# Performance work log

Measured on AMD Instinct MI355X. Metric: run time of the kernel, lower is better.

The kernel has to match this reference:

```python
import jax, jax.numpy as jnp
import numpy as np

NUM_ROWS = 125000
NUM_CACHE = 100000
EMB_DIMS = 128
ROW = [50, 50, 50]
EMB = [4, 4, 8]
R = [1, 32, 32, 1]
TT_IDX = jnp.array([2500, 50, 1], dtype=jnp.int64)  # strides from create_tt_idx_shape
NUM_IDX = 204800
NUM_BAGS = 4096


def setup_inputs() -> dict:
    key = jax.random.key(0)
    ks = jax.random.split(key, 8)
    indices = jax.random.randint(ks[0], (NUM_IDX,), 0, NUM_ROWS, dtype=jnp.int64)
    offsets = jnp.sort(jax.random.randint(ks[1], (NUM_BAGS + 1,), 0, NUM_IDX, dtype=jnp.int64))
    offsets = offsets.at[0].set(0).at[-1].set(NUM_IDX)
    cached_indices = jax.random.randint(ks[2], (NUM_IDX,), 0, NUM_CACHE, dtype=jnp.int64)
    cached_offsets = jnp.sort(jax.random.randint(ks[3], (NUM_BAGS + 1,), 0, NUM_IDX, dtype=jnp.int64))
    cached_offsets = cached_offsets.at[0].set(0).at[-1].set(NUM_IDX)
    sigma = 1.0 / np.sqrt(NUM_ROWS)
    core0 = jax.random.normal(ks[4], (ROW[0], R[0] * EMB[0] * R[1]), dtype=jnp.float32) * sigma
    core1 = jax.random.normal(ks[5], (ROW[1], R[1] * EMB[1] * R[2]), dtype=jnp.float32) * sigma
    core2 = jax.random.normal(ks[6], (ROW[2], R[2] * EMB[2] * R[3]), dtype=jnp.float32) * sigma
    cache_table = jax.random.normal(ks[7], (NUM_CACHE, EMB_DIMS), dtype=jnp.float32)
    return {"indices": indices, "offsets": offsets, "cached_indices": cached_indices,
            "cached_offsets": cached_offsets, "core0": core0, "core1": core1,
            "core2": core2, "cache_table": cache_table}


def _bag_ids(offsets, n):
    # bag id for each flat index position (include_last_offset convention)
    return jnp.searchsorted(offsets, jnp.arange(n, dtype=offsets.dtype), side='right') - 1


def reference(indices, offsets, cached_indices, cached_offsets, core0, core1, core2, cache_table):
    n = indices.shape[0]
    # TT index digit decomposition
    d0 = (indices // TT_IDX[0]) % ROW[0]
    d1 = (indices // TT_IDX[1]) % ROW[1]
    d2 = (indices // TT_IDX[2]) % ROW[2]
    g0 = core0[d0].reshape(n, EMB[0], R[1])            # [n, e0, r1]
    g1 = core1[d1].reshape(n, R[1], EMB[1], R[2])      # [n, r1, e1, r2]
    g2 = core2[d2].reshape(n, R[2], EMB[2])            # [n, r2, e2]
    t = jnp.einsum('nxr,nrys->nxys', g0, g1).reshape(n, EMB[0] * EMB[1], R[2])
    emb = jnp.einsum('nkr,nrz->nkz', t, g2).reshape(n, EMB_DIMS)  # [n, 128]
    seg_tt = _bag_ids(offsets, n)
    tt_bag = jax.ops.segment_sum(emb, seg_tt, num_segments=NUM_BAGS)
    seg_c = _bag_ids(cached_offsets, cached_indices.shape[0])
    cache_bag = jax.ops.segment_sum(cache_table[cached_indices], seg_c, num_segments=NUM_BAGS)
    return cache_bag + tt_bag
```

## Files before the change

### kernel.cpp

```cpp
#include <hip/hip_runtime.h>
#include <hip/hip_bf16.h>


#define PAIRS 2500
#define CHT 64
#define CHC 32

typedef unsigned int u32;
typedef unsigned short u16;

__device__ __forceinline__ float bfu(u16 u) { return __uint_as_float(((u32)u) << 16); }
__device__ __forceinline__ u16 f2bf(float x) {
  __hip_bfloat16 h = __float2bfloat16(x);
  return *reinterpret_cast<u16*>(&h);
}

__device__ __forceinline__ void gload_lds16(const void* g, void* l) {
  __builtin_amdgcn_global_load_lds(
      (const __attribute__((address_space(1))) u32*)g,
      (__attribute__((address_space(3))) u32*)l, 16, 0, 0);
}

__global__ __launch_bounds__(256) void chat_kernel(const float* __restrict__ core2,
                                                   float* __restrict__ chat) {
  const int d2 = blockIdx.x;
  const int tid = threadIdx.x;
  const int r = tid >> 3, z = tid & 7;
  chat[d2 * 288 + z * 36 + r] = core2[d2 * 256 + r * 8 + z];
}

__global__ __launch_bounds__(512, 4) void build_emb_kernel(
    const float* __restrict__ core0, const float* __restrict__ core1,
    const float* __restrict__ chat, u16* __restrict__ emb_t) {
  __shared__ float c0s[128];
  __shared__ float c1s[4096];
  __shared__ float ts[512];
  const int p = blockIdx.x;
  const int d0 = p / 50, d1 = p - d0 * 50;
  const int tid = threadIdx.x;

  {
    const float4* s1 = reinterpret_cast<const float4*>(core1 + (size_t)d1 * 4096);
    float4* dst = reinterpret_cast<float4*>(c1s);
    dst[tid] = s1[tid];
    dst[tid + 512] = s1[tid + 512];
    if (tid < 32)
      reinterpret_cast<float4*>(c0s)[tid] =
          reinterpret_cast<const float4*>(core0 + (size_t)d0 * 128)[tid];
  }
  __syncthreads();

  {
    const int kk = tid >> 5, s = tid & 31;
    const int x = kk >> 2, y = kk & 3;
    float acc = 0.f;
#pragma unroll
    for (int r = 0; r < 32; ++r)
      acc += c0s[x * 32 + r] * c1s[r * 128 + y * 32 + s];
    ts[kk * 32 + s] = acc;
  }
  __syncthreads();

  if (tid < 400) {
    const int d2 = tid >> 3, z = tid & 7;
    float4 c[8];
    const float4* cp = reinterpret_cast<const float4*>(chat + d2 * 288 + z * 36);
#pragma unroll
    for (int rq = 0; rq < 8; ++rq) c[rq] = cp[rq];
    const float4* t4 = reinterpret_cast<const float4*>(ts);
    u16* op = emb_t + (((size_t)(p * 50 + d2)) << 7) + z;
#pragma unroll
    for (int kk = 0; kk < 16; ++kk) {
      float s = 0.f;
#pragma unroll
      for (int rq = 0; rq < 8; ++rq) {
        const float4 tb = t4[kk * 8 + rq];
        s += tb.x * c[rq].x + tb.y * c[rq].y + tb.z * c[rq].z + tb.w * c[rq].w;
      }
      op[kk * 8] = f2bf(s);
    }
  }
}

__device__ __forceinline__ int bag_search(const int* __restrict__ offs,
                                          int nbags, int p) {
  int lo = 0, hi = nbags;
  while (hi - lo > 1) {
    int m = (lo + hi) >> 1;
    if (offs[m] <= p) lo = m; else hi = m;
  }
  return lo;
}

__global__ __launch_bounds__(256, 8) void sum_kernel(
    const int* __restrict__ indices, const int* __restrict__ offsets,
    const int* __restrict__ cached_indices, const int* __restrict__ cached_offsets,
    const float* __restrict__ cache_table, const u16* __restrict__ emb_t,
    float* __restrict__ out, int n, int nbags, int ntt_blocks) {
  __shared__ __align__(16) u16 sdat[CHT * 128];
  __shared__ int sidx[CHT];
  __shared__ int sbag[CHT];
  const int tid = threadIdx.x;
  const int bid = blockIdx.x;
  const int lane = tid & 63;
  const int w = tid >> 6;

  if (bid < ntt_blocks) {
    const int base = bid * CHT;
    const int count = min(CHT, n - base);
    if (tid < count) {
      sidx[tid] = indices[base + tid];
      sbag[tid] = bag_search(offsets, nbags, base + tid);
    }
    __syncthreads();
    if (count == CHT) {
      u32* ldsb = reinterpret_cast<u32*>(sdat);
#pragma unroll
      for (int j = 0; j < 4; ++j) {
        const int r4 = w * 16 + j * 4;
        const int row = r4 + (lane >> 4);
        const char* src = reinterpret_cast<const char*>(emb_t) +
                          (((size_t)sidx[row]) << 8) + ((lane & 15) << 4);
        gload_lds16(src, ldsb + r4 * 64);
      }
    } else {
      for (int r = w; r < count; r += 4) {
        reinterpret_cast<u32*>(sdat)[r * 64 + lane] =
            reinterpret_cast<const u32*>(emb_t)[(((size_t)sidx[r]) << 6) + lane];
      }
    }
    __syncthreads();
    const int k = tid & 127, h = tid >> 7;
    const int rlo = h * (CHT / 2);
    const int rhi = min(count, rlo + CHT / 2);
    float acc = 0.f;
    for (int i = rlo; i < rhi; ++i) {
      acc += bfu(sdat[i * 128 + k]);
      if (i + 1 == rhi || sbag[i + 1] != sbag[i]) {
        atomicAdd(out + (((size_t)sbag[i]) << 7) + k, acc);
        acc = 0.f;
      }
    }
  } else {
    const int cb = bid - ntt_blocks;
    const int base = cb * CHC;
    const int count = min(CHC, n - base);
    float* sfl = reinterpret_cast<float*>(sdat);
    if (tid < count) {
      sidx[tid] = cached_indices[base + tid];
      sbag[tid] = bag_search(cached_offsets, nbags, base + tid);
    }
    __syncthreads();
    if (count == CHC) {
#pragma unroll
      for (int j = 0; j < 4; ++j) {
        const int r2 = w * 8 + j * 2;
        const int row = r2 + (lane >> 5);
        const char* src = reinterpret_cast<const char*>(cache_table) +
                          (((size_t)sidx[row]) << 9) + ((lane & 31) << 4);
        gload_lds16(src, sfl + r2 * 128);
      }
    } else {
      for (int r = w; r < count; r += 4) {
        reinterpret_cast<float2*>(sfl + r * 128)[lane] =
            reinterpret_cast<const float2*>(cache_table + (((size_t)sidx[r]) << 7))[lane];
      }
    }
    __syncthreads();
    const int k = tid & 127, h = tid >> 7;
    const int rlo = h * (CHC / 2);
    const int rhi = min(count, rlo + CHC / 2);
    float acc = 0.f;
    for (int i = rlo; i < rhi; ++i) {
      acc += sfl[i * 128 + k];
      if (i + 1 == rhi || sbag[i + 1] != sbag[i]) {
        atomicAdd(out + (((size_t)sbag[i]) << 7) + k, acc);
        acc = 0.f;
      }
    }
  }
}

extern "C" void kernel_launch(void* const* d_in, const int* in_sizes, int n_in,
                              void* d_out, int out_size, void* d_ws, size_t ws_size,
                              hipStream_t stream) {
  const int* indices        = (const int*)d_in[0];
  const int* offsets        = (const int*)d_in[1];
  const int* cached_indices = (const int*)d_in[2];
  const int* cached_offsets = (const int*)d_in[3];
  const float* core0        = (const float*)d_in[4];
  const float* core1        = (const float*)d_in[5];
  const float* core2        = (const float*)d_in[6];
  const float* cache_table  = (const float*)d_in[7];
  float* out = (float*)d_out;

  const int n = in_sizes[0];
  const int nbags = in_sizes[1] - 1;

  u16* emb_t = (u16*)d_ws;
  float* chat = (float*)((char*)d_ws + 32000000);

  hipMemsetAsync(out, 0, (size_t)out_size * sizeof(float), stream);

  chat_kernel<<<50, 256, 0, stream>>>(core2, chat);
  build_emb_kernel<<<PAIRS, 512, 0, stream>>>(core0, core1, chat, emb_t);

  const int ntt = (n + CHT - 1) / CHT;
  const int nc  = (n + CHC - 1) / CHC;
  sum_kernel<<<ntt + nc, 256, 0, stream>>>(
      indices, offsets, cached_indices, cached_offsets, cache_table, emb_t,
      out, n, nbags, ntt);
}
```

Before: 165.9 us.

## Stage embedding tiles in swizzled LDS, overlap index loads with bag search

The build kernel now writes each pair's 50x128 bf16 block into a swizzled shared buffer and copies it out with coalesced 8-byte stores, replacing the strided 2-byte global stores. It also loads the core2 coefficients before the first barrier and removes the padded stride. The sum kernel reads indices straight from global memory so the gathers are issued before the bag binary search, precomputes a per-row bag/end flag, and has each thread accumulate two columns over quarter-chunks. This roughly doubles the number of atomics per row segment and adds extra shared memory and barriers in exchange for better store coalescing and load/search overlap.

Measured after the change: 193.6 us. 1.17x slower.

```diff
diff --git a/kernel.cpp b/kernel.cpp
--- a/kernel.cpp
+++ b/kernel.cpp
@@ -9,7 +9,8 @@
 typedef unsigned int u32;
 typedef unsigned short u16;
 
-__device__ __forceinline__ float bfu(u16 u) { return __uint_as_float(((u32)u) << 16); }
+__device__ __forceinline__ float bflo(u32 u) { return __uint_as_float(u << 16); }
+__device__ __forceinline__ float bfhi(u32 u) { return __uint_as_float(u & 0xffff0000u); }
 __device__ __forceinline__ u16 f2bf(float x) {
   __hip_bfloat16 h = __float2bfloat16(x);
   return *reinterpret_cast<u16*>(&h);
@@ -26,7 +27,7 @@
   const int d2 = blockIdx.x;
   const int tid = threadIdx.x;
   const int r = tid >> 3, z = tid & 7;
-  chat[d2 * 288 + z * 36 + r] = core2[d2 * 256 + r * 8 + z];
+  chat[d2 * 256 + z * 32 + r] = core2[d2 * 256 + r * 8 + z];
 }
 
 __global__ __launch_bounds__(512, 4) void build_emb_kernel(
@@ -35,6 +36,7 @@
   __shared__ float c0s[128];
   __shared__ float c1s[4096];
   __shared__ float ts[512];
+  __shared__ __align__(16) u16 ebuf[6400];
   const int p = blockIdx.x;
   const int d0 = p / 50, d1 = p - d0 * 50;
   const int tid = threadIdx.x;
@@ -48,6 +50,14 @@
       reinterpret_cast<float4*>(c0s)[tid] =
           reinterpret_cast<const float4*>(core0 + (size_t)d0 * 128)[tid];
   }
+
+  const int d2 = tid >> 3, z = tid & 7;
+  float4 c[8];
+  if (tid < 400) {
+    const float4* cp = reinterpret_cast<const float4*>(chat + d2 * 256 + z * 32);
+#pragma unroll
+    for (int rq = 0; rq < 8; ++rq) c[rq] = cp[rq];
+  }
   __syncthreads();
 
   {
@@ -62,13 +72,8 @@
   __syncthreads();
 
   if (tid < 400) {
-    const int d2 = tid >> 3, z = tid & 7;
-    float4 c[8];
-    const float4* cp = reinterpret_cast<const float4*>(chat + d2 * 288 + z * 36);
-#pragma unroll
-    for (int rq = 0; rq < 8; ++rq) c[rq] = cp[rq];
     const float4* t4 = reinterpret_cast<const float4*>(ts);
-    u16* op = emb_t + (((size_t)(p * 50 + d2)) << 7) + z;
+    const u32 sw = ((u32)(d2 & 7)) << 4;
 #pragma unroll
     for (int kk = 0; kk < 16; ++kk) {
       float s = 0.f;
@@ -77,7 +82,19 @@
         const float4 tb = t4[kk * 8 + rq];
         s += tb.x * c[rq].x + tb.y * c[rq].y + tb.z * c[rq].z + tb.w * c[rq].w;
       }
-      op[kk * 8] = f2bf(s);
+      const u32 byte = (u32)d2 * 256 + (u32)kk * 16 + (u32)z * 2;
+      *reinterpret_cast<u16*>(reinterpret_cast<char*>(ebuf) + (byte ^ sw)) = f2bf(s);
+    }
+  }
+  __syncthreads();
+
+  {
+    uint2* gdst = reinterpret_cast<uint2*>(emb_t + (size_t)p * 6400);
+    for (int e = tid; e < 1600; e += 512) {
+      const u32 byte = (u32)e * 8;
+      const u32 swb = byte ^ ((((byte >> 8) & 7)) << 4);
+      gdst[e] = *reinterpret_cast<const uint2*>(
+          reinterpret_cast<const char*>(ebuf) + swb);
     }
   }
 }
@@ -98,8 +115,8 @@
     const float* __restrict__ cache_table, const u16* __restrict__ emb_t,
     float* __restrict__ out, int n, int nbags, int ntt_blocks) {
   __shared__ __align__(16) u16 sdat[CHT * 128];
-  __shared__ int sidx[CHT];
   __shared__ int sbag[CHT];
+  __shared__ int sbb[CHT];
   const int tid = threadIdx.x;
   const int bid = blockIdx.x;
   const int lane = tid & 63;
@@ -108,37 +125,42 @@
   if (bid < ntt_blocks) {
     const int base = bid * CHT;
     const int count = min(CHT, n - base);
-    if (tid < count) {
-      sidx[tid] = indices[base + tid];
-      sbag[tid] = bag_search(offsets, nbags, base + tid);
-    }
-    __syncthreads();
     if (count == CHT) {
       u32* ldsb = reinterpret_cast<u32*>(sdat);
 #pragma unroll
       for (int j = 0; j < 4; ++j) {
         const int r4 = w * 16 + j * 4;
         const int row = r4 + (lane >> 4);
+        const int gidx = indices[base + row];
         const char* src = reinterpret_cast<const char*>(emb_t) +
-                          (((size_t)sidx[row]) << 8) + ((lane & 15) << 4);
+                          (((size_t)gidx) << 8) + ((lane & 15) << 4);
         gload_lds16(src, ldsb + r4 * 64);
       }
     } else {
       for (int r = w; r < count; r += 4) {
+        const int gidx = indices[base + r];
         reinterpret_cast<u32*>(sdat)[r * 64 + lane] =
-            reinterpret_cast<const u32*>(emb_t)[(((size_t)sidx[r]) << 6) + lane];
-      }
-    }
-    __syncthreads();
-    const int k = tid & 127, h = tid >> 7;
-    const int rlo = h * (CHT / 2);
-    const int rhi = min(count, rlo + CHT / 2);
-    float acc = 0.f;
+            reinterpret_cast<const u32*>(emb_t)[(((size_t)gidx) << 6) + lane];
+      }
+    }
+    if (tid < count) sbag[tid] = bag_search(offsets, nbags, base + tid);
+    __syncthreads();
+    if (tid < count)
+      sbb[tid] = (sbag[tid] << 1) |
+                 ((tid + 1 == count || sbag[tid + 1] != sbag[tid]) ? 1 : 0);
+    __syncthreads();
+
+    const int kp = tid & 63, h = tid >> 6;
+    const int rlo = h * 16, rhi = min(count, rlo + 16);
+    float a0 = 0.f, a1 = 0.f;
     for (int i = rlo; i < rhi; ++i) {
-      acc += bfu(sdat[i * 128 + k]);
-      if (i + 1 == rhi || sbag[i + 1] != sbag[i]) {
-        atomicAdd(out + (((size_t)sbag[i]) << 7) + k, acc);
-        acc = 0.f;
+      const u32 v = *reinterpret_cast<const u32*>(sdat + (size_t)i * 128 + kp * 2);
+      const int bb = sbb[i];
+      a0 += bflo(v); a1 += bfhi(v);
+      if ((bb & 1) || (i + 1 == rhi)) {
+        float* o = out + (((size_t)(bb >> 1)) << 7) + kp * 2;
+        atomicAdd(o, a0); atomicAdd(o + 1, a1);
+        a0 = 0.f; a1 = 0.f;
       }
     }
   } else {
@@ -146,36 +168,41 @@
     const int base = cb * CHC;
     const int count = min(CHC, n - base);
     float* sfl = reinterpret_cast<float*>(sdat);
-    if (tid < count) {
-      sidx[tid] = cached_indices[base + tid];
-      sbag[tid] = bag_search(cached_offsets, nbags, base + tid);
-    }
-    __syncthreads();
     if (count == CHC) {
 #pragma unroll
       for (int j = 0; j < 4; ++j) {
         const int r2 = w * 8 + j * 2;
         const int row = r2 + (lane >> 5);
+        const int gidx = cached_indices[base + row];
         const char* src = reinterpret_cast<const char*>(cache_table) +
-                          (((size_t)sidx[row]) << 9) + ((lane & 31) << 4);
+                          (((size_t)gidx) << 9) + ((lane & 31) << 4);
         gload_lds16(src, sfl + r2 * 128);
       }
     } else {
       for (int r = w; r < count; r += 4) {
+        const int gidx = cached_indices[base + r];
         reinterpret_cast<float2*>(sfl + r * 128)[lane] =
-            reinterpret_cast<const float2*>(cache_table + (((size_t)sidx[r]) << 7))[lane];
-      }
-    }
-    __syncthreads();
-    const int k = tid & 127, h = tid >> 7;
-    const int rlo = h * (CHC / 2);
-    const int rhi = min(count, rlo + CHC / 2);
-    float acc = 0.f;
+            reinterpret_cast<const float2*>(cache_table + (((size_t)gidx) << 7))[lane];
+      }
+    }
+    if (tid < count) sbag[tid] = bag_search(cached_offsets, nbags, base + tid);
+    __syncthreads();
+    if (tid < count)
+      sbb[tid] = (sbag[tid] << 1) |
+                 ((tid + 1 == count || sbag[tid + 1] != sbag[tid]) ? 1 : 0);
+    __syncthreads();
+
+    const int kp = tid & 63, h = tid >> 6;
+    const int rlo = h * 8, rhi = min(count, rlo + 8);
+    float a0 = 0.f, a1 = 0.f;
     for (int i = rlo; i < rhi; ++i) {
-      acc += sfl[i * 128 + k];
-      if (i + 1 == rhi || sbag[i + 1] != sbag[i]) {
-        atomicAdd(out + (((size_t)sbag[i]) << 7) + k, acc);
-        acc = 0.f;
+      const float2 v = *reinterpret_cast<const float2*>(sfl + (size_t)i * 128 + kp * 2);
+      const int bb = sbb[i];
+      a0 += v.x; a1 += v.y;
+      if ((bb & 1) || (i + 1 == rhi)) {
+        float* o = out + (((size_t)(bb >> 1)) << 7) + kp * 2;
+        atomicAdd(o, a0); atomicAdd(o + 1, a1);
+        a0 = 0.f; a1 = 0.f;
       }
     }
   }
```

## Restructure emb build kernel to 128 threads with register-blocked outputs and packed stores

Applied to the files above, without the earlier changes.

The block size of the TT embedding build kernel drops from 512 to 128 threads, and each thread now computes more work. In the first contraction each thread produces four outputs with float4 LDS reads. In the second contraction each thread computes four z outputs and writes them as packed bf16 uint2 stores instead of scattered 2-byte stores. The core2 transpose layout changes from a padded stride of 36 to a dense stride of 32. The goal is fewer LDS reads and wider global writes, at the cost of more registers per thread and only 100 of 128 threads active in the output phase.

Measured after the change: 171.8 us. 1.04x slower.

```diff
diff --git a/kernel.cpp b/kernel.cpp
--- a/kernel.cpp
+++ b/kernel.cpp
@@ -13,6 +13,9 @@
 __device__ __forceinline__ u16 f2bf(float x) {
   __hip_bfloat16 h = __float2bfloat16(x);
   return *reinterpret_cast<u16*>(&h);
+}
+__device__ __forceinline__ u32 pack2bf(float lo, float hi) {
+  return ((u32)f2bf(hi) << 16) | (u32)f2bf(lo);
 }
 
 __device__ __forceinline__ void gload_lds16(const void* g, void* l) {
@@ -26,10 +29,10 @@
   const int d2 = blockIdx.x;
   const int tid = threadIdx.x;
   const int r = tid >> 3, z = tid & 7;
-  chat[d2 * 288 + z * 36 + r] = core2[d2 * 256 + r * 8 + z];
-}
-
-__global__ __launch_bounds__(512, 4) void build_emb_kernel(
+  chat[d2 * 256 + z * 32 + r] = core2[d2 * 256 + tid];
+}
+
+__global__ __launch_bounds__(128) void build_emb_kernel(
     const float* __restrict__ core0, const float* __restrict__ core1,
     const float* __restrict__ chat, u16* __restrict__ emb_t) {
   __shared__ float c0s[128];
@@ -39,11 +42,23 @@
   const int d0 = p / 50, d1 = p - d0 * 50;
   const int tid = threadIdx.x;
 
+  const int d2 = tid >> 1, zg = tid & 1;
+  float4 c[4][8];
+  if (tid < 100) {
+#pragma unroll
+    for (int j = 0; j < 4; ++j) {
+      const float4* cp =
+          reinterpret_cast<const float4*>(chat + d2 * 256 + (zg * 4 + j) * 32);
+#pragma unroll
+      for (int rq = 0; rq < 8; ++rq) c[j][rq] = cp[rq];
+    }
+  }
+
   {
     const float4* s1 = reinterpret_cast<const float4*>(core1 + (size_t)d1 * 4096);
     float4* dst = reinterpret_cast<float4*>(c1s);
-    dst[tid] = s1[tid];
-    dst[tid + 512] = s1[tid + 512];
+#pragma unroll
+    for (int i = 0; i < 8; ++i) dst[tid + i * 128] = s1[tid + i * 128];
     if (tid < 32)
       reinterpret_cast<float4*>(c0s)[tid] =
           reinterpret_cast<const float4*>(core0 + (size_t)d0 * 128)[tid];
@@ -51,33 +66,34 @@
   __syncthreads();
 
   {
-    const int kk = tid >> 5, s = tid & 31;
+    const int kk = tid >> 3, s0 = (tid & 7) * 4;
     const int x = kk >> 2, y = kk & 3;
-    float acc = 0.f;
-#pragma unroll
-    for (int r = 0; r < 32; ++r)
-      acc += c0s[x * 32 + r] * c1s[r * 128 + y * 32 + s];
-    ts[kk * 32 + s] = acc;
+    float4 acc = make_float4(0.f, 0.f, 0.f, 0.f);
+#pragma unroll
+    for (int r = 0; r < 32; ++r) {
+      const float a = c0s[x * 32 + r];
+      const float4 b = *reinterpret_cast<const float4*>(c1s + r * 128 + y * 32 + s0);
+      acc.x += a * b.x; acc.y += a * b.y; acc.z += a * b.z; acc.w += a * b.w;
+    }
+    *reinterpret_cast<float4*>(ts + tid * 4) = acc;
   }
   __syncthreads();
 
-  if (tid < 400) {
-    const int d2 = tid >> 3, z = tid & 7;
-    float4 c[8];
-    const float4* cp = reinterpret_cast<const float4*>(chat + d2 * 288 + z * 36);
-#pragma unroll
-    for (int rq = 0; rq < 8; ++rq) c[rq] = cp[rq];
+  if (tid < 100) {
     const float4* t4 = reinterpret_cast<const float4*>(ts);
-    u16* op = emb_t + (((size_t)(p * 50 + d2)) << 7) + z;
+    uint2* orow = reinterpret_cast<uint2*>(emb_t + (((size_t)(p * 50 + d2)) << 7));
 #pragma unroll
     for (int kk = 0; kk < 16; ++kk) {
-      float s = 0.f;
+      float s0 = 0.f, s1 = 0.f, s2 = 0.f, s3 = 0.f;
 #pragma unroll
       for (int rq = 0; rq < 8; ++rq) {
         const float4 tb = t4[kk * 8 + rq];
-        s += tb.x * c[rq].x + tb.y * c[rq].y + tb.z * c[rq].z + tb.w * c[rq].w;
-      }
-      op[kk * 8] = f2bf(s);
+        s0 += tb.x * c[0][rq].x + tb.y * c[0][rq].y + tb.z * c[0][rq].z + tb.w * c[0][rq].w;
+        s1 += tb.x * c[1][rq].x + tb.y * c[1][rq].y + tb.z * c[1][rq].z + tb.w * c[1][rq].w;
+        s2 += tb.x * c[2][rq].x + tb.y * c[2][rq].y + tb.z * c[2][rq].z + tb.w * c[2][rq].w;
+        s3 += tb.x * c[3][rq].x + tb.y * c[3][rq].y + tb.z * c[3][rq].z + tb.w * c[3][rq].w;
+      }
+      orow[kk * 2 + zg] = make_uint2(pack2bf(s0, s1), pack2bf(s2, s3));
     }
   }
 }
@@ -203,7 +219,7 @@
   hipMemsetAsync(out, 0, (size_t)out_size * sizeof(float), stream);
 
   chat_kernel<<<50, 256, 0, stream>>>(core2, chat);
-  build_emb_kernel<<<PAIRS, 512, 0, stream>>>(core0, core1, chat, emb_t);
+  build_emb_kernel<<<PAIRS, 128, 0, stream>>>(core0, core1, chat, emb_t);
 
   const int ntt = (n + CHT - 1) / CHT;
   const int nc  = (n + CHC - 1) / CHC;
```
